# Optimization experiments

Hardware: AMD Instinct MI355X
Metric: run time of the kernel (lower is better)

Reference implementation:

```python
import jax, jax.numpy as jnp
import numpy as np

B, LEADS, T = 256, 12, 2250
ENC_DIM = 768           # encoder.width
LATENT = 128            # latent_dim
K = 512                 # num_embeddings
COMMIT = 0.1            # commitment_cost
IN_DIM = LEADS * T      # 27000


def setup_inputs() -> dict:
    key = jax.random.key(0)
    ks = jax.random.split(key, 9)
    s = lambda d: 1.0 / np.sqrt(d)
    return {
        "x": jax.random.normal(ks[0], (B, LEADS, T), dtype=jnp.float32),
        # frozen pretrained encoder, modeled as a linear projection (stop_gradient in reference)
        "W_enc": jax.random.normal(ks[1], (IN_DIM, ENC_DIM), dtype=jnp.float32) * s(IN_DIM),
        # to_latent
        "W_lat": jax.random.normal(ks[2], (ENC_DIM, LATENT), dtype=jnp.float32) * s(ENC_DIM),
        "b_lat": jnp.zeros((LATENT,), dtype=jnp.float32),
        # VQ codebook: torch.rand - 0.5  -> uniform(-0.5, 0.5)
        "codebook": jax.random.uniform(ks[3], (K, LATENT), dtype=jnp.float32, minval=-0.5, maxval=0.5),
        # decoder: Linear(LATENT, ENC_DIM) -> ReLU -> Linear(ENC_DIM, IN_DIM)
        "W_d1": jax.random.normal(ks[4], (LATENT, ENC_DIM), dtype=jnp.float32) * s(LATENT),
        "b_d1": jnp.zeros((ENC_DIM,), dtype=jnp.float32),
        "W_d2": jax.random.normal(ks[5], (ENC_DIM, IN_DIM), dtype=jnp.float32) * s(ENC_DIM),
        "b_d2": jnp.zeros((IN_DIM,), dtype=jnp.float32),
    }


def _vq(z, codebook):
    # z: [B, D]; codebook: [K, D]
    # distances = |z|^2 + |e|^2 - 2 z e^T   -> [B, K]
    d = (jnp.sum(z * z, axis=1, keepdims=True)
         + jnp.sum(codebook * codebook, axis=1)
         - 2.0 * jnp.matmul(z, codebook.T))
    idx = jnp.argmin(d, axis=1)                 # [B]
    quant = codebook[idx]                       # gather [B, D]
    e_latent = jnp.mean((jax.lax.stop_gradient(quant) - z) ** 2)
    q_latent = jnp.mean((quant - jax.lax.stop_gradient(z)) ** 2)
    loss = q_latent + COMMIT * e_latent
    quant_st = z + jax.lax.stop_gradient(quant - z)   # straight-through
    return quant_st, loss, idx


def reference(x, W_enc, W_lat, b_lat, codebook, W_d1, b_d1, W_d2, b_d2):
    # frozen encoder (requires_grad=False / torch.no_grad)
    features = jax.lax.stop_gradient(x.reshape(x.shape[0], -1) @ W_enc)   # [B, ENC_DIM]
    z = features @ W_lat + b_lat                                          # [B, LATENT]
    z_q, vq_loss, indices = _vq(z, codebook)
    h = jax.nn.relu(z_q @ W_d1 + b_d1)
    x_recon = (h @ W_d2 + b_d2).reshape(-1, LEADS, T)                     # [B, 12, 2250]
    recon_loss = jnp.mean((x_recon - x) ** 2)
    return x_recon, recon_loss + vq_loss, vq_loss, indices
```

## Files before the change

### kernel.cpp

```cpp
#include <hip/hip_runtime.h>
#include <hip/hip_bf16.h>

#define IN_DIM   27000
#define ENC_DIM  768
#define LATENT   128
#define K_CODES  512
#define BATCH    256
#define ZCH      288
#define NZC      94
#define NWC      211
#define BN_R     128
#define NRB      211
#define PADK     40
#define PADK2    72
#define NKT      24

#define OUT_WCTH_US   0
#define OUT_WCTL_US   (128*IN_DIM)
#define OUT_ZPART_F   (128*IN_DIM)

#define WS_Z      0
#define WS_QUANT  (WS_Z + BATCH*LATENT)
#define WS_IDX    (WS_QUANT + BATCH*LATENT)
#define WS_VQPART (WS_IDX + BATCH)
#define WS_RECON  (WS_VQPART + BATCH)
#define WS_HBF    (WS_RECON + 1024)
#define WS_WLH    (WS_HBF + 49152)
#define WS_WLL    (WS_WLH + 49152)

typedef unsigned short ushort_t;
typedef __attribute__((ext_vector_type(4))) float f32x4;
typedef __attribute__((ext_vector_type(8))) short short8x;
typedef __attribute__((ext_vector_type(4))) short short4x;

__device__ __forceinline__ ushort_t bf16_rne(float f) {
    unsigned u = __float_as_uint(f);
    unsigned r = 0x7FFFu + ((u >> 16) & 1u);
    return (ushort_t)((u + r) >> 16);
}
__device__ __forceinline__ void split_f32(float v, ushort_t& h, ushort_t& l) {
    unsigned u  = __float_as_uint(v);
    unsigned uh = u & 0xFFFF0000u;
    h = (ushort_t)(uh >> 16);
    l = bf16_rne(v - __uint_as_float(uh));
}
__device__ __forceinline__ void lds_barrier() {
    asm volatile("s_waitcnt lgkmcnt(0)\n\ts_barrier" ::: "memory");
}

__global__ __launch_bounds__(256) void k_prep(const float* __restrict__ Wlat,
                                              ushort_t* __restrict__ wlh,
                                              ushort_t* __restrict__ wll) {
    const int i4 = blockIdx.x * 256 + threadIdx.x;
    const int k  = i4 >> 5;
    const int n4 = (i4 & 31) * 4;
    float4 v = *(const float4*)(Wlat + (size_t)k * LATENT + n4);
    float vv[4] = {v.x, v.y, v.z, v.w};
#pragma unroll
    for (int j = 0; j < 4; j++) {
        ushort_t h, l;
        split_f32(vv[j], h, l);
        wlh[(size_t)(n4 + j) * ENC_DIM + k] = h;
        wll[(size_t)(n4 + j) * ENC_DIM + k] = l;
    }
}

__global__ __launch_bounds__(512) void k_wc(const float* __restrict__ Wenc,
                                            const ushort_t* __restrict__ wlh,
                                            const ushort_t* __restrict__ wll,
                                            ushort_t* __restrict__ wcth,
                                            ushort_t* __restrict__ wctl) {
    __shared__ ushort_t Bh[2][128][PADK2], Bl[2][128][PADK2];
    const int t = threadIdx.x, lane = t & 63, wid = t >> 6;
    const int lrow = lane & 15, kg = lane >> 4;
    const int half = wid >> 2, w8 = wid & 3;
    const int m0 = blockIdx.x * 128;
    int arow = m0 + half * 64 + w8 * 16 + lrow; if (arow > IN_DIM - 1) arow = IN_DIM - 1;
    const float* aptr = Wenc + (size_t)arow * ENC_DIM + kg * 8;
    const int bn = t >> 2, bkc = (t & 3) * 16;
    const size_t bbase = (size_t)bn * ENC_DIM + bkc;

    f32x4 acc[8];
#pragma unroll
    for (int ni = 0; ni < 8; ni++) acc[ni] = (f32x4){0.f, 0.f, 0.f, 0.f};

    float av0[8], av1[8], av2[8], av3[8];
    short8x bhA[2], blA[2], bhB[2], blB[2];

#define WC_ALOAD(S, kt)                                                         \
    {                                                                           \
        *(float4*)&av##S[0] = *(const float4*)(aptr + (kt) * 32);               \
        *(float4*)&av##S[4] = *(const float4*)(aptr + (kt) * 32 + 4);           \
    }
#define WC_BLOADP(SET, kt0)                                                     \
    {                                                                           \
        const ushort_t* ph = wlh + bbase + (kt0) * 32;                          \
        const ushort_t* pl = wll + bbase + (kt0) * 32;                          \
        bh##SET[0] = *(const short8x*)ph;  bh##SET[1] = *(const short8x*)(ph + 8); \
        bl##SET[0] = *(const short8x*)pl;  bl##SET[1] = *(const short8x*)(pl + 8); \
    }
#define WC_BSTOREP(SET, BI)                                                     \
    {                                                                           \
        *(short8x*)&Bh[BI][bn][bkc]     = bh##SET[0];                           \
        *(short8x*)&Bh[BI][bn][bkc + 8] = bh##SET[1];                           \
        *(short8x*)&Bl[BI][bn][bkc]     = bl##SET[0];                           \
        *(short8x*)&Bl[BI][bn][bkc + 8] = bl##SET[1];                           \
    }
#define WC_MFMAT(S, BI, SUB)                                                    \
    {                                                                           \
        short8x ah, al;                                                         \
        _Pragma("unroll")                                                       \
        for (int i = 0; i < 8; i++) {                                           \
            ushort_t h, l; split_f32(av##S[i], h, l);                           \
            ah[i] = (short)h; al[i] = (short)l;                                 \
        }                                                                       \
        __builtin_amdgcn_s_setprio(1);                                          \
        _Pragma("unroll")                                                       \
        for (int ni = 0; ni < 8; ni++) {                                        \
            short8x bhf = *(const short8x*)&Bh[BI][ni * 16 + lrow][(SUB) * 32 + kg * 8]; \
            short8x blf = *(const short8x*)&Bl[BI][ni * 16 + lrow][(SUB) * 32 + kg * 8]; \
            acc[ni] = __builtin_amdgcn_mfma_f32_16x16x32_bf16(ah, bhf, acc[ni], 0, 0, 0); \
            acc[ni] = __builtin_amdgcn_mfma_f32_16x16x32_bf16(ah, blf, acc[ni], 0, 0, 0); \
            acc[ni] = __builtin_amdgcn_mfma_f32_16x16x32_bf16(al, bhf, acc[ni], 0, 0, 0); \
        }                                                                       \
        __builtin_amdgcn_s_setprio(0);                                          \
    }

    WC_ALOAD(0, 0) WC_ALOAD(1, 1)
    WC_BLOADP(B, 0)
    WC_BSTOREP(B, 0)
    WC_BLOADP(A, 2)
    lds_barrier();

    for (int j = 0; j < NKT / 4; j++) {
        const int kt0 = 4 * j;
        if (kt0 + 2 < NKT) { WC_ALOAD(2, kt0 + 2) WC_ALOAD(3, kt0 + 3) }
        if (kt0 + 4 < NKT) WC_BLOADP(B, kt0 + 4)
        WC_MFMAT(0, 0, 0)
        WC_MFMAT(1, 0, 1)
        if (kt0 + 2 < NKT) WC_BSTOREP(A, 1)
        lds_barrier();
        if (kt0 + 4 < NKT) { WC_ALOAD(0, kt0 + 4) WC_ALOAD(1, kt0 + 5) }
        if (kt0 + 6 < NKT) WC_BLOADP(A, kt0 + 6)
        if (kt0 + 2 < NKT) { WC_MFMAT(2, 1, 0) WC_MFMAT(3, 1, 1) }
        if (kt0 + 4 < NKT) WC_BSTOREP(B, 0)
        lds_barrier();
    }
#undef WC_ALOAD
#undef WC_BLOADP
#undef WC_BSTOREP
#undef WC_MFMAT

    const int rowb = m0 + half * 64 + w8 * 16 + kg * 4;
    if (rowb < IN_DIM) {
#pragma unroll
        for (int ni = 0; ni < 8; ni++) {
            const int col = ni * 16 + lrow;
            short4x h4, l4;
#pragma unroll
            for (int r = 0; r < 4; r++) {
                ushort_t h, l; split_f32(acc[ni][r], h, l);
                h4[r] = (short)h; l4[r] = (short)l;
            }
            *(short4x*)(wcth + (size_t)col * IN_DIM + rowb) = h4;
            *(short4x*)(wctl + (size_t)col * IN_DIM + rowb) = l4;
        }
    }
}

__global__ __launch_bounds__(256) void k_z(const float* __restrict__ x,
                                           const ushort_t* __restrict__ wcth,
                                           const ushort_t* __restrict__ wctl,
                                           float* __restrict__ zpart) {
    __shared__ ushort_t Ah[2][64][PADK], Al[2][64][PADK];
    __shared__ ushort_t Bh[2][128][PADK], Bl[2][128][PADK];
    const int t = threadIdx.x, lane = t & 63, w = t >> 6;
    const int lrow = lane & 15, kg = lane >> 4;
    const int m0 = blockIdx.x * 64;
    const int c  = blockIdx.y;
    const int kb = c * ZCH;
    const int k_end = min(IN_DIM, kb + ZCH);
    const int nt = (k_end - kb + 31) >> 5;

    const int a_row = t >> 3, a_kq = t & 7;
    const int b_n   = t >> 2, b_ck = t & 3;

    float4  areg0[2], areg1[2];
    short8x bhreg0[2], blreg0[2], bhreg1[2], blreg1[2];

    f32x4 acc[8];
#pragma unroll
    for (int ni = 0; ni < 8; ni++) acc[ni] = (f32x4){0.f, 0.f, 0.f, 0.f};

#define Z_LOAD(S, kt)                                                           \
    {                                                                           \
        const int k0_ = kb + (kt) * 32;                                         \
        _Pragma("unroll")                                                       \
        for (int p = 0; p < 2; p++) {                                           \
            const int kk = k0_ + a_kq * 4;                                      \
            if (kk < k_end) {                                                   \
                const int r = m0 + a_row + p * 32;                              \
                areg##S[p] = *(const float4*)(x + (size_t)r * IN_DIM + kk);     \
            } else {                                                            \
                areg##S[p] = (float4){0.f, 0.f, 0.f, 0.f};                      \
            }                                                                   \
        }                                                                       \
        _Pragma("unroll")                                                       \
        for (int p = 0; p < 2; p++) {                                           \
            const int kk = k0_ + b_ck * 8;                                      \
            if (kk < k_end) {                                                   \
                const size_t bo = (size_t)(b_n + p * 64) * IN_DIM + kk;         \
                bhreg##S[p] = *(const short8x*)(wcth + bo);                     \
                blreg##S[p] = *(const short8x*)(wctl + bo);                     \
            } else {                                                            \
                short8x zz = {0, 0, 0, 0, 0, 0, 0, 0};                          \
                bhreg##S[p] = zz; blreg##S[p] = zz;                             \
            }                                                                   \
        }                                                                       \
    }
#define Z_STORE(S, BI)                                                          \
    {                                                                           \
        _Pragma("unroll")                                                       \
        for (int p = 0; p < 2; p++) {                                           \
            const int row = a_row + p * 32;                                     \
            float vv[4] = {areg##S[p].x, areg##S[p].y, areg##S[p].z, areg##S[p].w}; \
            short4x h4, l4;                                                     \
            _Pragma("unroll")                                                   \
            for (int i = 0; i < 4; i++) {                                       \
                ushort_t h, l; split_f32(vv[i], h, l);                          \
                h4[i] = (short)h; l4[i] = (short)l;                             \
            }                                                                   \
            *(short4x*)&Ah[BI][row][a_kq * 4] = h4;                             \
            *(short4x*)&Al[BI][row][a_kq * 4] = l4;                             \
        }                                                                       \
        _Pragma("unroll")                                                       \
        for (int p = 0; p < 2; p++) {                                           \
            const int n = b_n + p * 64;                                         \
            *(short8x*)&Bh[BI][n][b_ck * 8] = bhreg##S[p];                      \
            *(short8x*)&Bl[BI][n][b_ck * 8] = blreg##S[p];                      \
        }                                                                       \
    }
#define Z_MFMA(BI)                                                              \
    {                                                                           \
        short8x ah = *(const short8x*)&Ah[BI][w * 16 + lrow][kg * 8];           \
        short8x al = *(const short8x*)&Al[BI][w * 16 + lrow][kg * 8];           \
        __builtin_amdgcn_s_setprio(1);                                          \
        _Pragma("unroll")                                                       \
        for (int ni = 0; ni < 8; ni++) {                                        \
            short8x bhf = *(const short8x*)&Bh[BI][ni * 16 + lrow][kg * 8];     \
            short8x blf = *(const short8x*)&Bl[BI][ni * 16 + lrow][kg * 8];     \
            acc[ni] = __builtin_amdgcn_mfma_f32_16x16x32_bf16(ah, bhf, acc[ni], 0, 0, 0); \
            acc[ni] = __builtin_amdgcn_mfma_f32_16x16x32_bf16(ah, blf, acc[ni], 0, 0, 0); \
            acc[ni] = __builtin_amdgcn_mfma_f32_16x16x32_bf16(al, bhf, acc[ni], 0, 0, 0); \
        }                                                                       \
        __builtin_amdgcn_s_setprio(0);                                          \
    }

    Z_LOAD(0, 0)
    if (nt > 1) Z_LOAD(1, 1)
    Z_STORE(0, 0)
    lds_barrier();

    for (int kt = 0; kt < nt; kt += 2) {
        if (kt + 2 < nt) Z_LOAD(0, kt + 2)
        Z_MFMA(0)
        if (kt + 1 < nt) Z_STORE(1, 1)
        lds_barrier();
        if (kt + 1 < nt) {
            if (kt + 3 < nt) Z_LOAD(1, kt + 3)
            Z_MFMA(1)
            if (kt + 2 < nt) Z_STORE(0, 0)
            lds_barrier();
        }
    }
#undef Z_LOAD
#undef Z_STORE
#undef Z_MFMA

    float* zp = zpart + (size_t)c * (BATCH * LATENT);
    const int rowb = m0 + w * 16 + kg * 4;
#pragma unroll
    for (int ni = 0; ni < 8; ni++) {
        const int col = ni * 16 + lrow;
#pragma unroll
        for (int r = 0; r < 4; r++)
            zp[(size_t)(rowb + r) * LATENT + col] = acc[ni][r];
    }
}

__global__ __launch_bounds__(256) void k_zred(const float* __restrict__ zpart,
                                              const float* __restrict__ blat,
                                              float* __restrict__ z) {
    const int o = blockIdx.x * 256 + threadIdx.x;
    float s = blat[o & (LATENT - 1)];
    for (int c = 0; c < NZC; c++) s += zpart[(size_t)c * (BATCH * LATENT) + o];
    z[o] = s;
}

__global__ __launch_bounds__(256) void k_vq(const float* __restrict__ z,
                                            const float* __restrict__ cb,
                                            float* __restrict__ quant,
                                            int* __restrict__ idx_out,
                                            float* __restrict__ vqpart) {
    __shared__ float zs[LATENT];
    __shared__ float ds_[256];
    __shared__ int   is_[256];
    const int b = blockIdx.x, t = threadIdx.x;
    if (t < LATENT) zs[t] = z[b * LATENT + t];
    __syncthreads();

    float best_d = 3.4e38f; int best_i = 0;
#pragma unroll
    for (int rep = 0; rep < 2; rep++) {
        const int k = t + rep * 256;
        const float* e = cb + (size_t)k * LATENT;
        float acc = 0.f;
#pragma unroll 4
        for (int d = 0; d < LATENT; d += 4) {
            float4 ev = *(const float4*)(e + d);
            float d0 = zs[d]   - ev.x;
            float d1 = zs[d+1] - ev.y;
            float d2 = zs[d+2] - ev.z;
            float d3 = zs[d+3] - ev.w;
            acc += d0*d0 + d1*d1 + d2*d2 + d3*d3;
        }
        if (acc < best_d) { best_d = acc; best_i = k; }
    }
    ds_[t] = best_d; is_[t] = best_i;
    __syncthreads();
    for (int s = 128; s > 0; s >>= 1) {
        if (t < s) {
            float od = ds_[t+s]; int oi = is_[t+s];
            if (od < ds_[t] || (od == ds_[t] && oi < is_[t])) { ds_[t] = od; is_[t] = oi; }
        }
        __syncthreads();
    }
    const int best = is_[0];
    if (t == 0) idx_out[b] = best;

    float sq = 0.f;
    if (t < LATENT) {
        float q = cb[(size_t)best * LATENT + t];
        quant[b * LATENT + t] = q;
        float dd = q - zs[t];
        sq = dd * dd;
    }
    __syncthreads();
    ds_[t] = sq;
    __syncthreads();
    for (int s = 128; s > 0; s >>= 1) {
        if (t < s) ds_[t] += ds_[t+s];
        __syncthreads();
    }
    if (t == 0) vqpart[b] = ds_[0];
}

__global__ __launch_bounds__(256) void k_h(const float* __restrict__ quant,
                                           const float* __restrict__ Wd1,
                                           const float* __restrict__ bd1,
                                           ushort_t* __restrict__ hfrag) {
    const int bid = blockIdx.x, t = threadIdx.x;
    const int row = bid / 3;
    const int col = (bid % 3) * 256 + t;
    float acc = bd1[col];
    const float* q = quant + row * LATENT;
#pragma unroll 8
    for (int k = 0; k < LATENT; k++)
        acc = fmaf(q[k], Wd1[(size_t)k * ENC_DIM + col], acc);
    const int mt = row >> 4, lrow = row & 15;
    const int kt = col >> 5, kg = (col & 31) >> 3, j = col & 7;
    hfrag[((size_t)(mt * NKT + kt) * 64 + kg * 16 + lrow) * 8 + j] =
        bf16_rne(fmaxf(acc, 0.f));
}

__global__ __launch_bounds__(512) void k_recon_mfma(const ushort_t* __restrict__ hfrag,
                                                    const float* __restrict__ Wd2,
                                                    const float* __restrict__ bd2,
                                                    const float* __restrict__ x,
                                                    float* __restrict__ out,
                                                    float* __restrict__ reconpart) {
    __shared__ ushort_t Bts[2][BN_R][PADK];
    __shared__ float red[512];
    const int t = threadIdx.x, lane = t & 63, wid = t >> 6;
    const int lrow = lane & 15, kg = lane >> 4;
    const int n0 = blockIdx.x * BN_R;

    const int b_n   = t & 127;
    const int b_kq  = t >> 7;
    const bool bvalid = (n0 + b_n) < IN_DIM;
    const ushort_t* afrag0 = hfrag + ((size_t)(wid * 2 + 0) * NKT * 64 + lane) * 8;
    const ushort_t* afrag1 = hfrag + ((size_t)(wid * 2 + 1) * NKT * 64 + lane) * 8;

    f32x4 acc[2][8];
#pragma unroll
    for (int mi = 0; mi < 2; mi++)
#pragma unroll
        for (int ni = 0; ni < 8; ni++) acc[mi][ni] = (f32x4){0.f, 0.f, 0.f, 0.f};

    short8x a0[2], a1[2], a2[2], a3[2];
    float   bregs0[8], bregs1[8], bregs2[8], bregs3[8];

#define R_ALOAD(S, kt)                                                          \
    {                                                                           \
        a##S[0] = *(const short8x*)(afrag0 + (size_t)(kt) * 512);               \
        a##S[1] = *(const short8x*)(afrag1 + (size_t)(kt) * 512);               \
    }
#define R_BLOAD(S, kt)                                                          \
    {                                                                           \
        if (bvalid) {                                                           \
            const float* wp = Wd2 + (size_t)((kt) * 32 + b_kq * 8) * IN_DIM + n0 + b_n; \
            _Pragma("unroll")                                                   \
            for (int j = 0; j < 8; j++) bregs##S[j] = wp[(size_t)j * IN_DIM];   \
        } else {                                                                \
            _Pragma("unroll")                                                   \
            for (int j = 0; j < 8; j++) bregs##S[j] = 0.f;                      \
        }                                                                       \
    }
#define R_BSTORE(S, BI)                                                         \
    {                                                                           \
        short8x bb;                                                             \
        _Pragma("unroll")                                                       \
        for (int j = 0; j < 8; j++) bb[j] = (short)bf16_rne(bregs##S[j]);       \
        *(short8x*)&Bts[BI][b_n][b_kq * 8] = bb;                                \
    }
#define R_MFMA(S, BI)                                                           \
    {                                                                           \
        __builtin_amdgcn_s_setprio(1);                                          \
        _Pragma("unroll")                                                       \
        for (int ni = 0; ni < 8; ni++) {                                        \
            short8x b_ = *(const short8x*)&Bts[BI][ni * 16 + lrow][kg * 8];     \
            acc[0][ni] = __builtin_amdgcn_mfma_f32_16x16x32_bf16(a##S[0], b_, acc[0][ni], 0, 0, 0); \
            acc[1][ni] = __builtin_amdgcn_mfma_f32_16x16x32_bf16(a##S[1], b_, acc[1][ni], 0, 0, 0); \
        }                                                                       \
        __builtin_amdgcn_s_setprio(0);                                          \
    }

    R_ALOAD(0, 0) R_BLOAD(0, 0)
    R_ALOAD(1, 1) R_BLOAD(1, 1)
    R_ALOAD(2, 2) R_BLOAD(2, 2)
    R_BSTORE(0, 0)
    lds_barrier();

    for (int kt0 = 0; kt0 < NKT; kt0 += 4) {
        if (kt0 + 3 < NKT) { R_ALOAD(3, kt0 + 3) R_BLOAD(3, kt0 + 3) }
        R_MFMA(0, 0)
        if (kt0 + 1 < NKT) R_BSTORE(1, 1)
        lds_barrier();
        if (kt0 + 4 < NKT) { R_ALOAD(0, kt0 + 4) R_BLOAD(0, kt0 + 4) }
        R_MFMA(1, 1)
        if (kt0 + 2 < NKT) R_BSTORE(2, 0)
        lds_barrier();
        if (kt0 + 5 < NKT) { R_ALOAD(1, kt0 + 5) R_BLOAD(1, kt0 + 5) }
        R_MFMA(2, 0)
        if (kt0 + 3 < NKT) R_BSTORE(3, 1)
        lds_barrier();
        if (kt0 + 6 < NKT) { R_ALOAD(2, kt0 + 6) R_BLOAD(2, kt0 + 6) }
        R_MFMA(3, 1)
        if (kt0 + 4 < NKT) R_BSTORE(0, 0)
        lds_barrier();
    }
#undef R_ALOAD
#undef R_BLOAD
#undef R_BSTORE
#undef R_MFMA

    float lsq = 0.f;
#pragma unroll
    for (int mi = 0; mi < 2; mi++) {
        const int rowb = wid * 32 + mi * 16 + kg * 4;
#pragma unroll
        for (int ni = 0; ni < 8; ni++) {
            const int col = n0 + ni * 16 + lrow;
            if (col < IN_DIM) {
                const float bb = bd2[col];
#pragma unroll
                for (int r = 0; r < 4; r++) {
                    const int row = rowb + r;
                    float v = acc[mi][ni][r] + bb;
                    float e = v - x[(size_t)row * IN_DIM + col];
                    lsq += e * e;
                    out[(size_t)row * IN_DIM + col] = v;
                }
            }
        }
    }

    red[t] = lsq;
    __syncthreads();
    for (int s = 256; s > 0; s >>= 1) {
        if (t < s) red[t] += red[t + s];
        __syncthreads();
    }
    if (t == 0) reconpart[blockIdx.x] = red[0];
}

__global__ __launch_bounds__(256) void k_final(const float* __restrict__ reconpart,
                                               const float* __restrict__ vqpart,
                                               const int* __restrict__ idx,
                                               float* __restrict__ out,
                                               long long obase) {
    __shared__ float red[256];
    const int t = threadIdx.x;
    float s = 0.f;
    for (int i = t; i < NRB; i += 256) s += reconpart[i];
    red[t] = s;
    __syncthreads();
    for (int st = 128; st > 0; st >>= 1) {
        if (t < st) red[t] += red[t + st];
        __syncthreads();
    }
    const float recon_sum = red[0];
    __syncthreads();
    red[t] = vqpart[t];
    __syncthreads();
    for (int st = 128; st > 0; st >>= 1) {
        if (t < st) red[t] += red[t + st];
        __syncthreads();
    }
    const float vq_sum = red[0];
    if (t == 0) {
        float recon_loss = recon_sum / (float)((size_t)BATCH * IN_DIM);
        float vq_loss = 1.1f * vq_sum / (float)(BATCH * LATENT);
        out[obase + 0] = recon_loss + vq_loss;
        out[obase + 1] = vq_loss;
    }
    out[obase + 2 + t] = (float)idx[t];
}

extern "C" void kernel_launch(void* const* d_in, const int* in_sizes, int n_in,
                              void* d_out, int out_size, void* d_ws, size_t ws_size,
                              hipStream_t stream) {
    int ix = 0, iwe = 1, iwl = 2, ibl = 3, icb = 4, iwd1 = 5, ibd1 = 6, iwd2 = 7, ibd2 = 8;
    if (n_in == 9 && in_sizes[0] != BATCH * IN_DIM) {
        int p20[2] = {1, 7}, n20 = 0, p98[2] = {2, 5}, n98 = 0;
        for (int i = 0; i < 9; i++) {
            const int s = in_sizes[i];
            if      (s == BATCH * IN_DIM)    ix = i;
            else if (s == LATENT)            ibl = i;
            else if (s == K_CODES * LATENT)  icb = i;
            else if (s == ENC_DIM)           ibd1 = i;
            else if (s == IN_DIM)            ibd2 = i;
            else if (s == IN_DIM * ENC_DIM)  { if (n20 < 2) p20[n20++] = i; }
            else if (s == ENC_DIM * LATENT)  { if (n98 < 2) p98[n98++] = i; }
        }
        iwd2 = p20[0]; iwe = p20[1];
        iwd1 = p98[0]; iwl = p98[1];
    }
    const float* x    = (const float*)d_in[ix];
    const float* Wenc = (const float*)d_in[iwe];
    const float* Wlat = (const float*)d_in[iwl];
    const float* blat = (const float*)d_in[ibl];
    const float* cb   = (const float*)d_in[icb];
    const float* Wd1  = (const float*)d_in[iwd1];
    const float* bd1  = (const float*)d_in[ibd1];
    const float* Wd2  = (const float*)d_in[iwd2];
    const float* bd2  = (const float*)d_in[ibd2];

    float* out = (float*)d_out;
    ushort_t* wcth  = (ushort_t*)d_out + OUT_WCTH_US;
    ushort_t* wctl  = (ushort_t*)d_out + OUT_WCTL_US;
    float*    zpart = out + OUT_ZPART_F;

    float* ws            = (float*)d_ws;
    float* z             = ws + WS_Z;
    float* quant         = ws + WS_QUANT;
    int*   idxp          = (int*)(ws + WS_IDX);
    float* vqpart        = ws + WS_VQPART;
    float* reconpart     = ws + WS_RECON;
    ushort_t* hfrag      = (ushort_t*)(ws + WS_HBF);
    ushort_t* wlh        = (ushort_t*)(ws + WS_WLH);
    ushort_t* wll        = (ushort_t*)(ws + WS_WLL);

    const long long obase = (long long)out_size - 258;

    k_prep      <<<96, 256, 0, stream>>>(Wlat, wlh, wll);
    k_wc        <<<NWC, 512, 0, stream>>>(Wenc, wlh, wll, wcth, wctl);
    k_z         <<<dim3(4, NZC), 256, 0, stream>>>(x, wcth, wctl, zpart);
    k_zred      <<<128, 256, 0, stream>>>(zpart, blat, z);
    k_vq        <<<BATCH, 256, 0, stream>>>(z, cb, quant, idxp, vqpart);
    k_h         <<<768, 256, 0, stream>>>(quant, Wd1, bd1, hfrag);
    k_recon_mfma<<<NRB, 512, 0, stream>>>(hfrag, Wd2, bd2, x, out, reconpart);
    k_final     <<<1, 256, 0, stream>>>(reconpart, vqpart, idxp, out, obase);
}
```

Baseline: 130.6 us.

## Fuse W_enc·W_lat product with x projection into one encoder kernel

Merges the combined-weight kernel and the x-times-combined-weight kernel into a single kernel. Each block computes a 128-row slice of W_enc·W_lat, keeps it in LDS as split bf16 hi/lo, and immediately multiplies it against the matching 128-column slice of x for all 256 batch rows. This removes the global round trip of the 27000x128 combined weight and one kernel launch. In exchange the split-K partial sums grow from 94 to 211 slices, which adds traffic and work to the reduction kernel, and the partial buffer is placed in the output region with the last slice redirected to workspace.

```diff
diff --git a/kernel.cpp b/kernel.cpp
--- a/kernel.cpp
+++ b/kernel.cpp
@@ -6,18 +6,16 @@
 #define LATENT   128
 #define K_CODES  512
 #define BATCH    256
-#define ZCH      288
-#define NZC      94
 #define NWC      211
 #define BN_R     128
 #define NRB      211
 #define PADK     40
 #define PADK2    72
+#define PADW     136
 #define NKT      24
-
-#define OUT_WCTH_US   0
-#define OUT_WCTL_US   (128*IN_DIM)
-#define OUT_ZPART_F   (128*IN_DIM)
+#define NCH      211
+
+#define OUT_ZPART_F   0
 
 #define WS_Z      0
 #define WS_QUANT  (WS_Z + BATCH*LATENT)
@@ -27,6 +25,7 @@
 #define WS_HBF    (WS_RECON + 1024)
 #define WS_WLH    (WS_HBF + 49152)
 #define WS_WLL    (WS_WLH + 49152)
+#define WS_ZLAST  (WS_WLL + 49152)
 
 typedef unsigned short ushort_t;
 typedef __attribute__((ext_vector_type(4))) float f32x4;
@@ -65,12 +64,15 @@
     }
 }
 
-__global__ __launch_bounds__(512) void k_wc(const float* __restrict__ Wenc,
-                                            const ushort_t* __restrict__ wlh,
-                                            const ushort_t* __restrict__ wll,
-                                            ushort_t* __restrict__ wcth,
-                                            ushort_t* __restrict__ wctl) {
+__global__ __launch_bounds__(512) void k_enc(const float* __restrict__ Wenc,
+                                             const ushort_t* __restrict__ wlh,
+                                             const ushort_t* __restrict__ wll,
+                                             const float* __restrict__ x,
+                                             float* __restrict__ zpart,
+                                             float* __restrict__ zlast) {
     __shared__ ushort_t Bh[2][128][PADK2], Bl[2][128][PADK2];
+    ushort_t* WcHi = &Bh[0][0][0];
+    ushort_t* WcLo = &Bl[0][0][0];
     const int t = threadIdx.x, lane = t & 63, wid = t >> 6;
     const int lrow = lane & 15, kg = lane >> 4;
     const int half = wid >> 2, w8 = wid & 3;
@@ -151,8 +153,27 @@
 #undef WC_BSTOREP
 #undef WC_MFMAT
 
-    const int rowb = m0 + half * 64 + w8 * 16 + kg * 4;
-    if (rowb < IN_DIM) {
+    const float* xp0 = x + (size_t)(wid * 32 + lrow) * IN_DIM + m0;
+    const float* xp1 = xp0 + (size_t)16 * IN_DIM;
+    float axvX[16], axvY[16];
+#define ZXLOAD(SET, kt2)                                                        \
+    {                                                                           \
+        const int kloc = (kt2) * 32 + kg * 8;                                   \
+        if (m0 + kloc < IN_DIM) {                                               \
+            *(float4*)&axv##SET[0]  = *(const float4*)(xp0 + kloc);             \
+            *(float4*)&axv##SET[4]  = *(const float4*)(xp0 + kloc + 4);         \
+            *(float4*)&axv##SET[8]  = *(const float4*)(xp1 + kloc);             \
+            *(float4*)&axv##SET[12] = *(const float4*)(xp1 + kloc + 4);         \
+        } else {                                                                \
+            _Pragma("unroll")                                                   \
+            for (int i = 0; i < 16; i++) axv##SET[i] = 0.f;                     \
+        }                                                                       \
+    }
+    ZXLOAD(X, 0)
+    ZXLOAD(Y, 1)
+
+    {
+        const int rowk = half * 64 + w8 * 16 + kg * 4;
 #pragma unroll
         for (int ni = 0; ni < 8; ni++) {
             const int col = ni * 16 + lrow;
@@ -162,138 +183,75 @@
                 ushort_t h, l; split_f32(acc[ni][r], h, l);
                 h4[r] = (short)h; l4[r] = (short)l;
             }
-            *(short4x*)(wcth + (size_t)col * IN_DIM + rowb) = h4;
-            *(short4x*)(wctl + (size_t)col * IN_DIM + rowb) = l4;
+            *(short4x*)&WcHi[(size_t)col * PADW + rowk] = h4;
+            *(short4x*)&WcLo[(size_t)col * PADW + rowk] = l4;
         }
     }
-}
-
-__global__ __launch_bounds__(256) void k_z(const float* __restrict__ x,
-                                           const ushort_t* __restrict__ wcth,
-                                           const ushort_t* __restrict__ wctl,
-                                           float* __restrict__ zpart) {
-    __shared__ ushort_t Ah[2][64][PADK], Al[2][64][PADK];
-    __shared__ ushort_t Bh[2][128][PADK], Bl[2][128][PADK];
-    const int t = threadIdx.x, lane = t & 63, w = t >> 6;
-    const int lrow = lane & 15, kg = lane >> 4;
-    const int m0 = blockIdx.x * 64;
-    const int c  = blockIdx.y;
-    const int kb = c * ZCH;
-    const int k_end = min(IN_DIM, kb + ZCH);
-    const int nt = (k_end - kb + 31) >> 5;
-
-    const int a_row = t >> 3, a_kq = t & 7;
-    const int b_n   = t >> 2, b_ck = t & 3;
-
-    float4  areg0[2], areg1[2];
-    short8x bhreg0[2], blreg0[2], bhreg1[2], blreg1[2];
-
-    f32x4 acc[8];
-#pragma unroll
-    for (int ni = 0; ni < 8; ni++) acc[ni] = (f32x4){0.f, 0.f, 0.f, 0.f};
-
-#define Z_LOAD(S, kt)                                                           \
-    {                                                                           \
-        const int k0_ = kb + (kt) * 32;                                         \
+    lds_barrier();
+
+    f32x4 acc2[2][8];
+#pragma unroll
+    for (int mi = 0; mi < 2; mi++)
+#pragma unroll
+        for (int ni = 0; ni < 8; ni++) acc2[mi][ni] = (f32x4){0.f, 0.f, 0.f, 0.f};
+
+#define ZMFMA(SET, kt2)                                                         \
+    {                                                                           \
+        short8x ah0, al0, ah1, al1;                                             \
         _Pragma("unroll")                                                       \
-        for (int p = 0; p < 2; p++) {                                           \
-            const int kk = k0_ + a_kq * 4;                                      \
-            if (kk < k_end) {                                                   \
-                const int r = m0 + a_row + p * 32;                              \
-                areg##S[p] = *(const float4*)(x + (size_t)r * IN_DIM + kk);     \
-            } else {                                                            \
-                areg##S[p] = (float4){0.f, 0.f, 0.f, 0.f};                      \
-            }                                                                   \
-        }                                                                       \
-        _Pragma("unroll")                                                       \
-        for (int p = 0; p < 2; p++) {                                           \
-            const int kk = k0_ + b_ck * 8;                                      \
-            if (kk < k_end) {                                                   \
-                const size_t bo = (size_t)(b_n + p * 64) * IN_DIM + kk;         \
-                bhreg##S[p] = *(const short8x*)(wcth + bo);                     \
-                blreg##S[p] = *(const short8x*)(wctl + bo);                     \
-            } else {                                                            \
-                short8x zz = {0, 0, 0, 0, 0, 0, 0, 0};                          \
-                bhreg##S[p] = zz; blreg##S[p] = zz;                             \
-            }                                                                   \
-        }                                                                       \
-    }
-#define Z_STORE(S, BI)                                                          \
-    {                                                                           \
-        _Pragma("unroll")                                                       \
-        for (int p = 0; p < 2; p++) {                                           \
-            const int row = a_row + p * 32;                                     \
-            float vv[4] = {areg##S[p].x, areg##S[p].y, areg##S[p].z, areg##S[p].w}; \
-            short4x h4, l4;                                                     \
-            _Pragma("unroll")                                                   \
-            for (int i = 0; i < 4; i++) {                                       \
-                ushort_t h, l; split_f32(vv[i], h, l);                          \
-                h4[i] = (short)h; l4[i] = (short)l;                             \
-            }                                                                   \
-            *(short4x*)&Ah[BI][row][a_kq * 4] = h4;                             \
-            *(short4x*)&Al[BI][row][a_kq * 4] = l4;                             \
-        }                                                                       \
-        _Pragma("unroll")                                                       \
-        for (int p = 0; p < 2; p++) {                                           \
-            const int n = b_n + p * 64;                                         \
-            *(short8x*)&Bh[BI][n][b_ck * 8] = bhreg##S[p];                      \
-            *(short8x*)&Bl[BI][n][b_ck * 8] = blreg##S[p];                      \
-        }                                                                       \
-    }
-#define Z_MFMA(BI)                                                              \
-    {                                                                           \
-        short8x ah = *(const short8x*)&Ah[BI][w * 16 + lrow][kg * 8];           \
-        short8x al = *(const short8x*)&Al[BI][w * 16 + lrow][kg * 8];           \
+        for (int i = 0; i < 8; i++) {                                           \
+            ushort_t h, l;                                                      \
+            split_f32(axv##SET[i], h, l);     ah0[i] = (short)h; al0[i] = (short)l; \
+            split_f32(axv##SET[8 + i], h, l); ah1[i] = (short)h; al1[i] = (short)l; \
+        }                                                                       \
         __builtin_amdgcn_s_setprio(1);                                          \
         _Pragma("unroll")                                                       \
         for (int ni = 0; ni < 8; ni++) {                                        \
-            short8x bhf = *(const short8x*)&Bh[BI][ni * 16 + lrow][kg * 8];     \
-            short8x blf = *(const short8x*)&Bl[BI][ni * 16 + lrow][kg * 8];     \
-            acc[ni] = __builtin_amdgcn_mfma_f32_16x16x32_bf16(ah, bhf, acc[ni], 0, 0, 0); \
-            acc[ni] = __builtin_amdgcn_mfma_f32_16x16x32_bf16(ah, blf, acc[ni], 0, 0, 0); \
-            acc[ni] = __builtin_amdgcn_mfma_f32_16x16x32_bf16(al, bhf, acc[ni], 0, 0, 0); \
+            const size_t bo = (size_t)(ni * 16 + lrow) * PADW + (kt2) * 32 + kg * 8; \
+            short8x bhf = *(const short8x*)&WcHi[bo];                           \
+            short8x blf = *(const short8x*)&WcLo[bo];                           \
+            acc2[0][ni] = __builtin_amdgcn_mfma_f32_16x16x32_bf16(ah0, bhf, acc2[0][ni], 0, 0, 0); \
+            acc2[0][ni] = __builtin_amdgcn_mfma_f32_16x16x32_bf16(ah0, blf, acc2[0][ni], 0, 0, 0); \
+            acc2[0][ni] = __builtin_amdgcn_mfma_f32_16x16x32_bf16(al0, bhf, acc2[0][ni], 0, 0, 0); \
+            acc2[1][ni] = __builtin_amdgcn_mfma_f32_16x16x32_bf16(ah1, bhf, acc2[1][ni], 0, 0, 0); \
+            acc2[1][ni] = __builtin_amdgcn_mfma_f32_16x16x32_bf16(ah1, blf, acc2[1][ni], 0, 0, 0); \
+            acc2[1][ni] = __builtin_amdgcn_mfma_f32_16x16x32_bf16(al1, bhf, acc2[1][ni], 0, 0, 0); \
         }                                                                       \
         __builtin_amdgcn_s_setprio(0);                                          \
     }
 
-    Z_LOAD(0, 0)
-    if (nt > 1) Z_LOAD(1, 1)
-    Z_STORE(0, 0)
-    lds_barrier();
-
-    for (int kt = 0; kt < nt; kt += 2) {
-        if (kt + 2 < nt) Z_LOAD(0, kt + 2)
-        Z_MFMA(0)
-        if (kt + 1 < nt) Z_STORE(1, 1)
-        lds_barrier();
-        if (kt + 1 < nt) {
-            if (kt + 3 < nt) Z_LOAD(1, kt + 3)
-            Z_MFMA(1)
-            if (kt + 2 < nt) Z_STORE(0, 0)
-            lds_barrier();
+    ZMFMA(X, 0)
+    ZXLOAD(X, 2)
+    ZMFMA(Y, 1)
+    ZXLOAD(Y, 3)
+    ZMFMA(X, 2)
+    ZMFMA(Y, 3)
+#undef ZXLOAD
+#undef ZMFMA
+
+    float* zp = (blockIdx.x == NCH - 1) ? zlast
+                                        : zpart + (size_t)blockIdx.x * (BATCH * LATENT);
+#pragma unroll
+    for (int mi = 0; mi < 2; mi++) {
+        const int rowb = wid * 32 + mi * 16 + kg * 4;
+#pragma unroll
+        for (int ni = 0; ni < 8; ni++) {
+            const int col = ni * 16 + lrow;
+#pragma unroll
+            for (int r = 0; r < 4; r++)
+                zp[(size_t)(rowb + r) * LATENT + col] = acc2[mi][ni][r];
         }
     }
-#undef Z_LOAD
-#undef Z_STORE
-#undef Z_MFMA
-
-    float* zp = zpart + (size_t)c * (BATCH * LATENT);
-    const int rowb = m0 + w * 16 + kg * 4;
-#pragma unroll
-    for (int ni = 0; ni < 8; ni++) {
-        const int col = ni * 16 + lrow;
-#pragma unroll
-        for (int r = 0; r < 4; r++)
-            zp[(size_t)(rowb + r) * LATENT + col] = acc[ni][r];
-    }
 }
 
 __global__ __launch_bounds__(256) void k_zred(const float* __restrict__ zpart,
+                                              const float* __restrict__ zlast,
                                               const float* __restrict__ blat,
                                               float* __restrict__ z) {
     const int o = blockIdx.x * 256 + threadIdx.x;
     float s = blat[o & (LATENT - 1)];
-    for (int c = 0; c < NZC; c++) s += zpart[(size_t)c * (BATCH * LATENT) + o];
+    for (int c = 0; c < NCH - 1; c++) s += zpart[(size_t)c * (BATCH * LATENT) + o];
+    s += zlast[o];
     z[o] = s;
 }
 
@@ -556,10 +514,8 @@
     const float* Wd2  = (const float*)d_in[iwd2];
     const float* bd2  = (const float*)d_in[ibd2];
 
-    float* out = (float*)d_out;
-    ushort_t* wcth  = (ushort_t*)d_out + OUT_WCTH_US;
-    ushort_t* wctl  = (ushort_t*)d_out + OUT_WCTL_US;
-    float*    zpart = out + OUT_ZPART_F;
+    float* out   = (float*)d_out;
+    float* zpart = out + OUT_ZPART_F;
 
     float* ws            = (float*)d_ws;
     float* z             = ws + WS_Z;
@@ -570,13 +526,13 @@
     ushort_t* hfrag      = (ushort_t*)(ws + WS_HBF);
     ushort_t* wlh        = (ushort_t*)(ws + WS_WLH);
     ushort_t* wll        = (ushort_t*)(ws + WS_WLL);
+    float* zlast         = ws + WS_ZLAST;
 
     const long long obase = (long long)out_size - 258;
 
     k_prep      <<<96, 256, 0, stream>>>(Wlat, wlh, wll);
-    k_wc        <<<NWC, 512, 0, stream>>>(Wenc, wlh, wll, wcth, wctl);
-    k_z         <<<dim3(4, NZC), 256, 0, stream>>>(x, wcth, wctl, zpart);
-    k_zred      <<<128, 256, 0, stream>>>(zpart, blat, z);
+    k_enc       <<<NWC, 512, 0, stream>>>(Wenc, wlh, wll, x, zpart, zlast);
+    k_zred      <<<128, 256, 0, stream>>>(zpart, zlast, blat, z);
     k_vq        <<<BATCH, 256, 0, stream>>>(z, cb, quant, idxp, vqpart);
     k_h         <<<768, 256, 0, stream>>>(quant, Wd1, bd1, hfrag);
     k_recon_mfma<<<NRB, 512, 0, stream>>>(hfrag, Wd2, bd2, x, out, reconpart);
```

Measured after the change: 107.3 us. 17.8% less time.
